# Kernel optimization log

Hardware: AMD Instinct MI355X
Metric: run time of the kernel (lower is better)

## Reference

```python
import jax, jax.numpy as jnp
import numpy as np

N, E = 10000, 320000
NF, HF = 256, 256  # input_nf/output_nf, hidden_nf
EPS = 1e-8


def setup_inputs() -> dict:
    key = jax.random.key(0)
    ks = jax.random.split(key, 20)
    h = jax.random.normal(ks[0], (N, NF), jnp.float32)
    coord = jax.random.normal(ks[1], (N, 3), jnp.float32)
    edge_index = jax.random.randint(ks[2], (2, E), 0, N, jnp.int32)

    def dense(k, fan_in, fan_out, scale=None):
        s = scale if scale is not None else 1.0 / np.sqrt(fan_in)
        W = jax.random.normal(k, (fan_in, fan_out), jnp.float32) * s
        b = jnp.zeros((fan_out,), jnp.float32)
        return W, b

    We1, be1 = dense(ks[3], 2 * NF + 1, HF)   # edge_mlp layer 1
    We2, be2 = dense(ks[4], HF, HF)           # edge_mlp layer 2
    Wn1, bn1 = dense(ks[5], HF + NF, HF)      # node_mlp layer 1
    Wn2, bn2 = dense(ks[6], HF, NF)           # node_mlp layer 2
    Wc1, bc1 = dense(ks[7], HF, HF)           # coord_mlp layer 1
    Wc2, bc2 = dense(ks[8], HF, 1, scale=0.001)  # coord_mlp final, tiny init (xavier gain=0.001)
    return dict(h=h, coord=coord, edge_index=edge_index,
                We1=We1, be1=be1, We2=We2, be2=be2,
                Wn1=Wn1, bn1=bn1, Wn2=Wn2, bn2=bn2,
                Wc1=Wc1, bc1=bc1, Wc2=Wc2, bc2=bc2)


def _segment_sum(data, seg_ids, num_segments):
    return jax.ops.segment_sum(data, seg_ids, num_segments=num_segments)


def reference(h, coord, edge_index, We1, be1, We2, be2, Wn1, bn1, Wn2, bn2, Wc1, bc1, Wc2, bc2):
    row, col = edge_index[0], edge_index[1]

    # coord2radial
    coord_diff = coord[row] - coord[col]                    # [E, 3]
    radial = jnp.sum(coord_diff ** 2, axis=1, keepdims=True)  # [E, 1]

    # edge model: MLP on [h_i, h_j, ||x_i - x_j||^2]
    edge_in = jnp.concatenate([h[row], h[col], radial], axis=1)  # [E, 2*NF+1]
    e = jax.nn.silu(edge_in @ We1 + be1)
    edge_feat = jax.nn.silu(e @ We2 + be2)                  # [E, HF]

    # coord model: coord_diff * coord_mlp(edge_feat), mean-aggregated
    c = jax.nn.silu(edge_feat @ Wc1 + bc1)
    trans = coord_diff * (c @ Wc2 + bc2)                    # [E, 3]
    agg_c = _segment_sum(trans, row, coord.shape[0])
    count = _segment_sum(jnp.ones_like(trans), row, coord.shape[0])
    coord_out = coord + agg_c / jnp.clip(count, 1.0)

    # node model: sum-aggregate edge features, concat with h, MLP
    agg_h = _segment_sum(edge_feat, row, h.shape[0])        # [N, HF]
    node_in = jnp.concatenate([h, agg_h], axis=1)           # [N, HF+NF]
    n = jax.nn.silu(node_in @ Wn1 + bn1)
    h_out = n @ Wn2 + bn2                                   # [N, NF]

    return h_out, coord_out
```

## Files before the change

### kernel.cpp

```cpp
#include <hip/hip_runtime.h>
#include <hip/hip_bf16.h>

typedef __bf16 bf16;
typedef __attribute__((ext_vector_type(8))) __bf16 bf16x8;
typedef __attribute__((ext_vector_type(4))) float f32x4;

static_assert(sizeof(bf16x8) == 16, "bf16x8 must be 16B");

constexpr int N_NODES = 10000;
constexpr int N_EDGES = 320000;
constexpr int KPAD    = 264;

__device__ __forceinline__ float silu_f(float x) { return x / (1.0f + __expf(-x)); }

__device__ __forceinline__ unsigned pk_bf16(float lo, float hi) {
  unsigned r;
  asm("v_cvt_pk_bf16_f32 %0, %1, %2" : "=v"(r) : "v"(lo), "v"(hi));
  return r;
}

__device__ __forceinline__ void mfmaT_k256(const bf16* __restrict__ WT, int wstride, int koff,
                                           const bf16* Albs, int w, int r, int q, f32x4 acc[4][4]) {
  for (int k0 = 0; k0 < 256; k0 += 32) {
    bf16x8 a[4], b[4];
#pragma unroll
    for (int mi = 0; mi < 4; ++mi)
      a[mi] = *(const bf16x8*)(WT + (size_t)(w * 64 + 16 * mi + r) * wstride + koff + k0 + q * 8);
#pragma unroll
    for (int ni = 0; ni < 4; ++ni)
      b[ni] = *(const bf16x8*)(Albs + (16 * ni + r) * KPAD + k0 + q * 8);
#pragma unroll
    for (int mi = 0; mi < 4; ++mi)
#pragma unroll
      for (int ni = 0; ni < 4; ++ni)
        acc[mi][ni] = __builtin_amdgcn_mfma_f32_16x16x32_bf16(a[mi], b[ni], acc[mi][ni], 0, 0, 0);
  }
}

__global__ __launch_bounds__(256) void prep_kernel(
    const float* __restrict__ h, const float* __restrict__ We1, const float* __restrict__ We2,
    const float* __restrict__ Wn1, const float* __restrict__ Wn2, const float* __restrict__ Wc1,
    const int* __restrict__ eidx,
    bf16* __restrict__ Hb, bf16* __restrict__ We1T, bf16* __restrict__ Wn1T,
    bf16* __restrict__ We2T, bf16* __restrict__ Wn2T, bf16* __restrict__ Wc1T,
    int* __restrict__ hist) {
  int bid = blockIdx.x, tid = threadIdx.x;
  if (bid < 10000) { int i = bid * 256 + tid; Hb[i] = (bf16)h[i]; return; }
  if (bid >= 11792) {
    int e = (bid - 11792) * 256 + tid;
    if (e < N_EDGES) atomicAdd(&hist[eidx[e]], 1);
    return;
  }
  int t = (bid - 10000) * 256 + tid;
  if (t < 131072) { int k = t >> 8, j = t & 255; We1T[j * 512 + k] = (bf16)We1[k * 256 + j]; return; }
  t -= 131072;
  if (t < 131072) { int k = t >> 8, j = t & 255; Wn1T[j * 512 + k] = (bf16)Wn1[k * 256 + j]; return; }
  t -= 131072;
  if (t < 65536) { int k = t >> 8, j = t & 255; We2T[j * 256 + k] = (bf16)We2[k * 256 + j]; return; }
  t -= 65536;
  if (t < 65536) { int k = t >> 8, j = t & 255; Wn2T[j * 256 + k] = (bf16)Wn2[k * 256 + j]; return; }
  t -= 65536;
  if (t < 65536) { int k = t >> 8, j = t & 255; Wc1T[j * 256 + k] = (bf16)Wc1[k * 256 + j]; return; }
}

__global__ __launch_bounds__(256) void scan_kernel(const int* __restrict__ hist,
                                                   int* __restrict__ base, int* __restrict__ cursor) {
  __shared__ int partial[256];
  int t = threadIdx.x;
  int s = 0;
  for (int i = 0; i < 40; ++i) { int idx = t * 40 + i; if (idx < N_NODES) s += hist[idx]; }
  partial[t] = s;
  __syncthreads();
  for (int d = 1; d < 256; d <<= 1) {
    int v = (t >= d) ? partial[t - d] : 0;
    __syncthreads();
    partial[t] += v;
    __syncthreads();
  }
  int run = partial[t] - s;
  for (int i = 0; i < 40; ++i) {
    int idx = t * 40 + i;
    if (idx < N_NODES) { base[idx] = run; cursor[idx] = run; run += hist[idx]; }
  }
}

__global__ __launch_bounds__(256) void scatter_kernel(const int* __restrict__ eidx, int* __restrict__ cursor,
                                                      int* __restrict__ rs, int* __restrict__ cs) {
  int e = blockIdx.x * 256 + threadIdx.x;
  if (e < N_EDGES) {
    int r = eidx[e], c = eidx[N_EDGES + e];
    int p = atomicAdd(&cursor[r], 1);
    rs[p] = r; cs[p] = c;
  }
}

__global__ __launch_bounds__(256, 2) void gemm_pq(const bf16* __restrict__ Hb,
                                                  const bf16* __restrict__ We1T,
                                                  const float* __restrict__ be1,
                                                  bf16* __restrict__ P, bf16* __restrict__ Q) {
  int tid = threadIdx.x, w = tid >> 6, lane = tid & 63, r = lane & 15, q = lane >> 4;
  int m0 = blockIdx.x * 64;
  int koff = blockIdx.y ? 256 : 0;
  bf16* OUT = blockIdx.y ? Q : P;
  bool addb = (blockIdx.y == 0);
  f32x4 acc[4][4];
#pragma unroll
  for (int mi = 0; mi < 4; ++mi)
#pragma unroll
    for (int ni = 0; ni < 4; ++ni) acc[mi][ni] = (f32x4){0.f, 0.f, 0.f, 0.f};

  for (int k0 = 0; k0 < 256; k0 += 32) {
    bf16x8 a[4], b[4];
#pragma unroll
    for (int mi = 0; mi < 4; ++mi)
      a[mi] = *(const bf16x8*)(We1T + (size_t)(w * 64 + 16 * mi + r) * 512 + koff + k0 + q * 8);
#pragma unroll
    for (int ni = 0; ni < 4; ++ni) {
      int m = m0 + 16 * ni + r; if (m > N_NODES - 1) m = N_NODES - 1;
      b[ni] = *(const bf16x8*)(Hb + (size_t)m * 256 + k0 + q * 8);
    }
#pragma unroll
    for (int mi = 0; mi < 4; ++mi)
#pragma unroll
      for (int ni = 0; ni < 4; ++ni)
        acc[mi][ni] = __builtin_amdgcn_mfma_f32_16x16x32_bf16(a[mi], b[ni], acc[mi][ni], 0, 0, 0);
  }
#pragma unroll
  for (int mi = 0; mi < 4; ++mi) {
    int ch = w * 64 + 16 * mi + 4 * q;
    float4 bv = addb ? *(const float4*)(be1 + ch) : (float4){0.f, 0.f, 0.f, 0.f};
#pragma unroll
    for (int ni = 0; ni < 4; ++ni) {
      int m = m0 + 16 * ni + r;
      if (m < N_NODES) {
        uint2 o;
        o.x = pk_bf16(acc[mi][ni][0] + bv.x, acc[mi][ni][1] + bv.y);
        o.y = pk_bf16(acc[mi][ni][2] + bv.z, acc[mi][ni][3] + bv.w);
        *(uint2*)(OUT + (size_t)m * 256 + ch) = o;
      }
    }
  }
}

__global__ __launch_bounds__(256, 4) void edge_kernel(
    const float* __restrict__ coord, const int* __restrict__ rs, const int* __restrict__ cs,
    const float* __restrict__ We1,
    const float* __restrict__ be2, const float* __restrict__ bc1,
    const float* __restrict__ Wc2, const float* __restrict__ bc2,
    const bf16* __restrict__ P, const bf16* __restrict__ Q,
    const bf16* __restrict__ We2T, const bf16* __restrict__ Wc1T,
    float* __restrict__ agg_h, float* __restrict__ agg_c) {
  __shared__ __align__(16) bf16 buf[64 * KPAD];
  __shared__ int s_row[64], s_col[64];
  __shared__ float s_rad[64], s_cd[64][3], s_part[64][4], s_scal[64];
  __shared__ int s_rs[65];
  __shared__ int s_nrun;

  int tid = threadIdx.x;
  int e0 = blockIdx.x * 64;
  int w = tid >> 6, lane = tid & 63, r = lane & 15, q = lane >> 4;

  if (tid < 64) {
    int e = e0 + tid;
    int ri = rs[e], ci = cs[e];
    s_row[tid] = ri; s_col[tid] = ci;
    float dx = coord[3 * ri + 0] - coord[3 * ci + 0];
    float dy = coord[3 * ri + 1] - coord[3 * ci + 1];
    float dz = coord[3 * ri + 2] - coord[3 * ci + 2];
    s_cd[tid][0] = dx; s_cd[tid][1] = dy; s_cd[tid][2] = dz;
    s_rad[tid] = dx * dx + dy * dy + dz * dz;
  }
  __syncthreads();

  if (tid < 64) {
    bool bnd = (tid == 0) || (s_row[tid] != s_row[tid - 1]);
    unsigned long long m = __ballot(bnd);
    int rank = __popcll(m & ((1ull << tid) - 1ull));
    if (bnd) s_rs[rank] = tid;
    if (tid == 0) { int R = __popcll(m); s_nrun = R; s_rs[R] = 64; }
  }

  {
    int off = (tid & 31) * 8;
    int esub = tid >> 5;
    float4 wa = *(const float4*)(We1 + 512 * 256 + off);
    float4 wb = *(const float4*)(We1 + 512 * 256 + off + 4);
#pragma unroll
    for (int p = 0; p < 8; ++p) {
      int e = p * 8 + esub;
      int ri = s_row[e], ci = s_col[e];
      bf16x8 pv = *(const bf16x8*)(P + (size_t)ri * 256 + off);
      bf16x8 qv = *(const bf16x8*)(Q + (size_t)ci * 256 + off);
      float rad = s_rad[e];
      float f0 = silu_f((float)pv[0] + (float)qv[0] + rad * wa.x);
      float f1 = silu_f((float)pv[1] + (float)qv[1] + rad * wa.y);
      float f2 = silu_f((float)pv[2] + (float)qv[2] + rad * wa.z);
      float f3 = silu_f((float)pv[3] + (float)qv[3] + rad * wa.w);
      float f4 = silu_f((float)pv[4] + (float)qv[4] + rad * wb.x);
      float f5 = silu_f((float)pv[5] + (float)qv[5] + rad * wb.y);
      float f6 = silu_f((float)pv[6] + (float)qv[6] + rad * wb.z);
      float f7 = silu_f((float)pv[7] + (float)qv[7] + rad * wb.w);
      uint4 o;
      o.x = pk_bf16(f0, f1); o.y = pk_bf16(f2, f3);
      o.z = pk_bf16(f4, f5); o.w = pk_bf16(f6, f7);
      *(uint4*)(buf + e * KPAD + off) = o;
    }
  }
  __syncthreads();

  {
    f32x4 acc[4][4];
#pragma unroll
    for (int mi = 0; mi < 4; ++mi)
#pragma unroll
      for (int ni = 0; ni < 4; ++ni) acc[mi][ni] = (f32x4){0.f, 0.f, 0.f, 0.f};
    mfmaT_k256(We2T, 256, 0, buf, w, r, q, acc);
    __syncthreads();
#pragma unroll
    for (int mi = 0; mi < 4; ++mi) {
      int ch = w * 64 + 16 * mi + 4 * q;
      float4 bv = *(const float4*)(be2 + ch);
#pragma unroll
      for (int ni = 0; ni < 4; ++ni) {
        int edge = 16 * ni + r;
        float f0 = silu_f(acc[mi][ni][0] + bv.x);
        float f1 = silu_f(acc[mi][ni][1] + bv.y);
        float f2 = silu_f(acc[mi][ni][2] + bv.z);
        float f3 = silu_f(acc[mi][ni][3] + bv.w);
        uint2 o; o.x = pk_bf16(f0, f1); o.y = pk_bf16(f2, f3);
        *(uint2*)(buf + edge * KPAD + ch) = o;
      }
    }
  }
  __syncthreads();

  f32x4 acc2[4][4];
#pragma unroll
  for (int mi = 0; mi < 4; ++mi)
#pragma unroll
    for (int ni = 0; ni < 4; ++ni) acc2[mi][ni] = (f32x4){0.f, 0.f, 0.f, 0.f};
  mfmaT_k256(Wc1T, 256, 0, buf, w, r, q, acc2);

  {
    int R = s_nrun;
    for (int rr = 0; rr < R; ++rr) {
      int st = s_rs[rr], en = s_rs[rr + 1];
      float s = 0.f;
      for (int e = st; e < en; ++e) s += (float)buf[e * KPAD + tid];
      atomicAdd(&agg_h[(size_t)s_row[st] * 256 + tid], s);
    }
  }

  {
    float p[4] = {0.f, 0.f, 0.f, 0.f};
#pragma unroll
    for (int mi = 0; mi < 4; ++mi) {
      int ch = w * 64 + 16 * mi + 4 * q;
      float4 bv = *(const float4*)(bc1 + ch);
      float4 wv = *(const float4*)(Wc2 + ch);
#pragma unroll
      for (int ni = 0; ni < 4; ++ni) {
        p[ni] += silu_f(acc2[mi][ni][0] + bv.x) * wv.x
               + silu_f(acc2[mi][ni][1] + bv.y) * wv.y
               + silu_f(acc2[mi][ni][2] + bv.z) * wv.z
               + silu_f(acc2[mi][ni][3] + bv.w) * wv.w;
      }
    }
#pragma unroll
    for (int ni = 0; ni < 4; ++ni) {
      float v = p[ni];
      v += __shfl_xor(v, 16, 64);
      v += __shfl_xor(v, 32, 64);
      if (q == 0) s_part[16 * ni + r][w] = v;
    }
  }
  __syncthreads();

  if (tid < 64)
    s_scal[tid] = s_part[tid][0] + s_part[tid][1] + s_part[tid][2] + s_part[tid][3] + bc2[0];
  __syncthreads();

  if (tid < 3) {
    int R = s_nrun;
    for (int rr = 0; rr < R; ++rr) {
      int st = s_rs[rr], en = s_rs[rr + 1];
      float s = 0.f;
      for (int e = st; e < en; ++e) s += s_cd[e][tid] * s_scal[e];
      atomicAdd(&agg_c[3 * s_row[st] + tid], s);
    }
  }
}

__global__ __launch_bounds__(256, 2) void node_kernel(
    const bf16* __restrict__ Hb, const float* __restrict__ agg_h,
    const int* __restrict__ hist, const float* __restrict__ coord, const float* __restrict__ agg_c,
    const bf16* __restrict__ Wn1T, const bf16* __restrict__ Wn2T,
    const float* __restrict__ bn1, const float* __restrict__ bn2,
    float* __restrict__ h_out, float* __restrict__ coord_out) {
  __shared__ __align__(16) bf16 buf[64 * KPAD];
  int tid = threadIdx.x, w = tid >> 6, lane = tid & 63, r = lane & 15, q = lane >> 4;
  int m0 = blockIdx.x * 64;

  if (tid < 64) {
    int m = m0 + tid;
    if (m < N_NODES) {
      float c = (float)hist[m]; if (c < 1.f) c = 1.f;
      coord_out[3 * m + 0] = coord[3 * m + 0] + agg_c[3 * m + 0] / c;
      coord_out[3 * m + 1] = coord[3 * m + 1] + agg_c[3 * m + 1] / c;
      coord_out[3 * m + 2] = coord[3 * m + 2] + agg_c[3 * m + 2] / c;
    }
  }

  f32x4 acc[4][4];
#pragma unroll
  for (int mi = 0; mi < 4; ++mi)
#pragma unroll
    for (int ni = 0; ni < 4; ++ni) acc[mi][ni] = (f32x4){0.f, 0.f, 0.f, 0.f};
  for (int k0 = 0; k0 < 256; k0 += 32) {
    bf16x8 a[4], b[4];
#pragma unroll
    for (int mi = 0; mi < 4; ++mi)
      a[mi] = *(const bf16x8*)(Wn1T + (size_t)(w * 64 + 16 * mi + r) * 512 + k0 + q * 8);
#pragma unroll
    for (int ni = 0; ni < 4; ++ni) {
      int m = m0 + 16 * ni + r; if (m > N_NODES - 1) m = N_NODES - 1;
      b[ni] = *(const bf16x8*)(Hb + (size_t)m * 256 + k0 + q * 8);
    }
#pragma unroll
    for (int mi = 0; mi < 4; ++mi)
#pragma unroll
      for (int ni = 0; ni < 4; ++ni)
        acc[mi][ni] = __builtin_amdgcn_mfma_f32_16x16x32_bf16(a[mi], b[ni], acc[mi][ni], 0, 0, 0);
  }
  for (int k0 = 0; k0 < 256; k0 += 32) {
    bf16x8 a[4], b[4];
#pragma unroll
    for (int mi = 0; mi < 4; ++mi)
      a[mi] = *(const bf16x8*)(Wn1T + (size_t)(w * 64 + 16 * mi + r) * 512 + 256 + k0 + q * 8);
#pragma unroll
    for (int ni = 0; ni < 4; ++ni) {
      int m = m0 + 16 * ni + r; if (m > N_NODES - 1) m = N_NODES - 1;
      const float* ap = agg_h + (size_t)m * 256 + k0 + q * 8;
      float4 u = *(const float4*)ap;
      float4 v = *(const float4*)(ap + 4);
      uint4 o;
      o.x = pk_bf16(u.x, u.y); o.y = pk_bf16(u.z, u.w);
      o.z = pk_bf16(v.x, v.y); o.w = pk_bf16(v.z, v.w);
      b[ni] = *(const bf16x8*)&o;
    }
#pragma unroll
    for (int mi = 0; mi < 4; ++mi)
#pragma unroll
      for (int ni = 0; ni < 4; ++ni)
        acc[mi][ni] = __builtin_amdgcn_mfma_f32_16x16x32_bf16(a[mi], b[ni], acc[mi][ni], 0, 0, 0);
  }
  __syncthreads();
#pragma unroll
  for (int mi = 0; mi < 4; ++mi) {
    int ch = w * 64 + 16 * mi + 4 * q;
    float4 bv = *(const float4*)(bn1 + ch);
#pragma unroll
    for (int ni = 0; ni < 4; ++ni) {
      int lm = 16 * ni + r;
      float f0 = silu_f(acc[mi][ni][0] + bv.x);
      float f1 = silu_f(acc[mi][ni][1] + bv.y);
      float f2 = silu_f(acc[mi][ni][2] + bv.z);
      float f3 = silu_f(acc[mi][ni][3] + bv.w);
      uint2 o; o.x = pk_bf16(f0, f1); o.y = pk_bf16(f2, f3);
      *(uint2*)(buf + lm * KPAD + ch) = o;
    }
  }
  __syncthreads();
  f32x4 acc2[4][4];
#pragma unroll
  for (int mi = 0; mi < 4; ++mi)
#pragma unroll
    for (int ni = 0; ni < 4; ++ni) acc2[mi][ni] = (f32x4){0.f, 0.f, 0.f, 0.f};
  mfmaT_k256(Wn2T, 256, 0, buf, w, r, q, acc2);
#pragma unroll
  for (int mi = 0; mi < 4; ++mi) {
    int ch = w * 64 + 16 * mi + 4 * q;
    float4 bv = *(const float4*)(bn2 + ch);
#pragma unroll
    for (int ni = 0; ni < 4; ++ni) {
      int m = m0 + 16 * ni + r;
      if (m < N_NODES) {
        float4 o;
        o.x = acc2[mi][ni][0] + bv.x;
        o.y = acc2[mi][ni][1] + bv.y;
        o.z = acc2[mi][ni][2] + bv.z;
        o.w = acc2[mi][ni][3] + bv.w;
        *(float4*)(h_out + (size_t)m * 256 + ch) = o;
      }
    }
  }
}

extern "C" void kernel_launch(void* const* d_in, const int* in_sizes, int n_in,
                              void* d_out, int out_size, void* d_ws, size_t ws_size,
                              hipStream_t stream) {
  const float* h     = (const float*)d_in[0];
  const float* coord = (const float*)d_in[1];
  const int*   eidx  = (const int*)d_in[2];
  const float* We1 = (const float*)d_in[3];
  const float* be1 = (const float*)d_in[4];
  const float* We2 = (const float*)d_in[5];
  const float* be2 = (const float*)d_in[6];
  const float* Wn1 = (const float*)d_in[7];
  const float* bn1 = (const float*)d_in[8];
  const float* Wn2 = (const float*)d_in[9];
  const float* bn2 = (const float*)d_in[10];
  const float* Wc1 = (const float*)d_in[11];
  const float* bc1 = (const float*)d_in[12];
  const float* Wc2 = (const float*)d_in[13];
  const float* bc2 = (const float*)d_in[14];

  char* ws = (char*)d_ws;
  float* agg_h = (float*)(ws + 0);
  float* agg_c = (float*)(ws + 10240000);
  int*   hist  = (int*)  (ws + 10360000);
  int*   base  = (int*)  (ws + 10400000);
  int*   cursor= (int*)  (ws + 10440000);
  int*   rs    = (int*)  (ws + 10480000);
  int*   cs    = (int*)  (ws + 11760000);
  bf16* Hb   = (bf16*)(ws + 13040000);
  bf16* P    = (bf16*)(ws + 18160000);
  bf16* Q    = (bf16*)(ws + 23280000);
  bf16* We1T = (bf16*)(ws + 28400000);
  bf16* Wn1T = (bf16*)(ws + 28662144);
  bf16* We2T = (bf16*)(ws + 28924288);
  bf16* Wn2T = (bf16*)(ws + 29055360);
  bf16* Wc1T = (bf16*)(ws + 29186432);

  float* h_out = (float*)d_out;
  float* coord_out = h_out + (size_t)N_NODES * 256;

  hipMemsetAsync(ws, 0, 10400000, stream);
  prep_kernel<<<13042, 256, 0, stream>>>(h, We1, We2, Wn1, Wn2, Wc1, eidx,
                                         Hb, We1T, Wn1T, We2T, Wn2T, Wc1T, hist);
  scan_kernel<<<1, 256, 0, stream>>>(hist, base, cursor);
  scatter_kernel<<<1250, 256, 0, stream>>>(eidx, cursor, rs, cs);
  gemm_pq<<<dim3(157, 2), 256, 0, stream>>>(Hb, We1T, be1, P, Q);
  edge_kernel<<<5000, 256, 0, stream>>>(coord, rs, cs, We1, be2, bc1, Wc2, bc2,
                                        P, Q, We2T, Wc1T, agg_h, agg_c);
  node_kernel<<<157, 256, 0, stream>>>(Hb, agg_h, hist, coord, agg_c,
                                       Wn1T, Wn2T, bn1, bn2, h_out, coord_out);
}
```

Baseline: 444.1 us.

## Shrink node GEMM tiles, vectorize weight transpose, fuse zeroing into prep

The node-side GEMMs (gemm_pq and node_kernel) now use 16-row tiles across 625 blocks instead of 64-row tiles across 157, so they fill more CUs on a 10000-node problem. Weight transposes write packed 8-element bf16 vectors. The large agg_h/agg_c memset moves into the prep kernel as float4 stores. The row/col arrays are packed into one int2 array. The scan stages hist in shared memory. SiLU uses a hardware reciprocal. Smaller tiles reduce weight reuse per block, and the bf16 transpose reads are strided.

```diff
diff --git a/kernel.cpp b/kernel.cpp
--- a/kernel.cpp
+++ b/kernel.cpp
@@ -11,7 +11,10 @@
 constexpr int N_EDGES = 320000;
 constexpr int KPAD    = 264;
 
-__device__ __forceinline__ float silu_f(float x) { return x / (1.0f + __expf(-x)); }
+__device__ __forceinline__ float rcp_f(float x) {
+  float r; asm("v_rcp_f32 %0, %1" : "=v"(r) : "v"(x)); return r;
+}
+__device__ __forceinline__ float silu_f(float x) { return x * rcp_f(1.0f + __expf(-x)); }
 
 __device__ __forceinline__ unsigned pk_bf16(float lo, float hi) {
   unsigned r;
@@ -35,6 +38,39 @@
       for (int ni = 0; ni < 4; ++ni)
         acc[mi][ni] = __builtin_amdgcn_mfma_f32_16x16x32_bf16(a[mi], b[ni], acc[mi][ni], 0, 0, 0);
   }
+}
+
+__device__ __forceinline__ void mfmaT_k256_b1(const bf16* __restrict__ WT, int wstride, int koff,
+                                              const bf16* Albs, int w, int r, int q, f32x4 acc[4]) {
+  for (int k0 = 0; k0 < 256; k0 += 32) {
+    bf16x8 a[4], b;
+    b = *(const bf16x8*)(Albs + r * KPAD + k0 + q * 8);
+#pragma unroll
+    for (int mi = 0; mi < 4; ++mi)
+      a[mi] = *(const bf16x8*)(WT + (size_t)(w * 64 + 16 * mi + r) * wstride + koff + k0 + q * 8);
+#pragma unroll
+    for (int mi = 0; mi < 4; ++mi)
+      acc[mi] = __builtin_amdgcn_mfma_f32_16x16x32_bf16(a[mi], b, acc[mi], 0, 0, 0);
+  }
+}
+
+__device__ __forceinline__ void transpose512(const float* __restrict__ W, bf16* __restrict__ WT,
+                                             int local, int tid) {
+  int tg = local * 256 + tid;
+  int j = tg >> 6, k0 = (tg & 63) * 8;
+  bf16x8 v;
+#pragma unroll
+  for (int i = 0; i < 8; ++i) v[i] = (bf16)W[(size_t)(k0 + i) * 256 + j];
+  *(bf16x8*)(WT + (size_t)j * 512 + k0) = v;
+}
+__device__ __forceinline__ void transpose256(const float* __restrict__ W, bf16* __restrict__ WT,
+                                             int local, int tid) {
+  int tg = local * 256 + tid;
+  int j = tg >> 5, k0 = (tg & 31) * 8;
+  bf16x8 v;
+#pragma unroll
+  for (int i = 0; i < 8; ++i) v[i] = (bf16)W[(size_t)(k0 + i) * 256 + j];
+  *(bf16x8*)(WT + (size_t)j * 256 + k0) = v;
 }
 
 __global__ __launch_bounds__(256) void prep_kernel(
@@ -43,32 +79,37 @@
     const int* __restrict__ eidx,
     bf16* __restrict__ Hb, bf16* __restrict__ We1T, bf16* __restrict__ Wn1T,
     bf16* __restrict__ We2T, bf16* __restrict__ Wn2T, bf16* __restrict__ Wc1T,
-    int* __restrict__ hist) {
+    int* __restrict__ hist, float4* __restrict__ zero_base) {
   int bid = blockIdx.x, tid = threadIdx.x;
   if (bid < 10000) { int i = bid * 256 + tid; Hb[i] = (bf16)h[i]; return; }
-  if (bid >= 11792) {
-    int e = (bid - 11792) * 256 + tid;
+  if (bid < 10224) {
+    int wb = bid - 10000;
+    if (wb < 64)       transpose512(We1, We1T, wb, tid);
+    else if (wb < 128) transpose512(Wn1, Wn1T, wb - 64, tid);
+    else if (wb < 160) transpose256(We2, We2T, wb - 128, tid);
+    else if (wb < 192) transpose256(Wn2, Wn2T, wb - 160, tid);
+    else               transpose256(Wc1, Wc1T, wb - 192, tid);
+    return;
+  }
+  if (bid < 11474) {
+    int e = (bid - 11474 + 1250) * 256 + tid - 1250 * 256;
+    e = (bid - 10224) * 256 + tid;
     if (e < N_EDGES) atomicAdd(&hist[eidx[e]], 1);
     return;
   }
-  int t = (bid - 10000) * 256 + tid;
-  if (t < 131072) { int k = t >> 8, j = t & 255; We1T[j * 512 + k] = (bf16)We1[k * 256 + j]; return; }
-  t -= 131072;
-  if (t < 131072) { int k = t >> 8, j = t & 255; Wn1T[j * 512 + k] = (bf16)Wn1[k * 256 + j]; return; }
-  t -= 131072;
-  if (t < 65536) { int k = t >> 8, j = t & 255; We2T[j * 256 + k] = (bf16)We2[k * 256 + j]; return; }
-  t -= 65536;
-  if (t < 65536) { int k = t >> 8, j = t & 255; Wn2T[j * 256 + k] = (bf16)Wn2[k * 256 + j]; return; }
-  t -= 65536;
-  if (t < 65536) { int k = t >> 8, j = t & 255; Wc1T[j * 256 + k] = (bf16)Wc1[k * 256 + j]; return; }
+  int z = (bid - 11474) * 256 + tid;
+  if (z < 647500) zero_base[z] = (float4){0.f, 0.f, 0.f, 0.f};
 }
 
 __global__ __launch_bounds__(256) void scan_kernel(const int* __restrict__ hist,
                                                    int* __restrict__ base, int* __restrict__ cursor) {
+  __shared__ int sh[10000];
   __shared__ int partial[256];
   int t = threadIdx.x;
+  for (int i = 0; i < 40; ++i) { int idx = i * 256 + t; if (idx < N_NODES) sh[idx] = hist[idx]; }
+  __syncthreads();
   int s = 0;
-  for (int i = 0; i < 40; ++i) { int idx = t * 40 + i; if (idx < N_NODES) s += hist[idx]; }
+  for (int i = 0; i < 40; ++i) { int idx = t * 40 + i; if (idx < N_NODES) s += sh[idx]; }
   partial[t] = s;
   __syncthreads();
   for (int d = 1; d < 256; d <<= 1) {
@@ -80,17 +121,22 @@
   int run = partial[t] - s;
   for (int i = 0; i < 40; ++i) {
     int idx = t * 40 + i;
-    if (idx < N_NODES) { base[idx] = run; cursor[idx] = run; run += hist[idx]; }
+    if (idx < N_NODES) { int hv = sh[idx]; sh[idx] = run; run += hv; }
+  }
+  __syncthreads();
+  for (int i = 0; i < 40; ++i) {
+    int idx = i * 256 + t;
+    if (idx < N_NODES) { int v = sh[idx]; base[idx] = v; cursor[idx] = v; }
   }
 }
 
 __global__ __launch_bounds__(256) void scatter_kernel(const int* __restrict__ eidx, int* __restrict__ cursor,
-                                                      int* __restrict__ rs, int* __restrict__ cs) {
+                                                      int2* __restrict__ rc) {
   int e = blockIdx.x * 256 + threadIdx.x;
   if (e < N_EDGES) {
     int r = eidx[e], c = eidx[N_EDGES + e];
     int p = atomicAdd(&cursor[r], 1);
-    rs[p] = r; cs[p] = c;
+    rc[p] = (int2){r, c};
   }
 }
 
@@ -99,51 +145,38 @@
                                                   const float* __restrict__ be1,
                                                   bf16* __restrict__ P, bf16* __restrict__ Q) {
   int tid = threadIdx.x, w = tid >> 6, lane = tid & 63, r = lane & 15, q = lane >> 4;
-  int m0 = blockIdx.x * 64;
+  int m0 = blockIdx.x * 16;
   int koff = blockIdx.y ? 256 : 0;
   bf16* OUT = blockIdx.y ? Q : P;
   bool addb = (blockIdx.y == 0);
-  f32x4 acc[4][4];
-#pragma unroll
-  for (int mi = 0; mi < 4; ++mi)
-#pragma unroll
-    for (int ni = 0; ni < 4; ++ni) acc[mi][ni] = (f32x4){0.f, 0.f, 0.f, 0.f};
+  f32x4 acc[4];
+#pragma unroll
+  for (int mi = 0; mi < 4; ++mi) acc[mi] = (f32x4){0.f, 0.f, 0.f, 0.f};
+  int m = m0 + r;
 
   for (int k0 = 0; k0 < 256; k0 += 32) {
-    bf16x8 a[4], b[4];
+    bf16x8 a[4], b;
+    b = *(const bf16x8*)(Hb + (size_t)m * 256 + k0 + q * 8);
 #pragma unroll
     for (int mi = 0; mi < 4; ++mi)
       a[mi] = *(const bf16x8*)(We1T + (size_t)(w * 64 + 16 * mi + r) * 512 + koff + k0 + q * 8);
 #pragma unroll
-    for (int ni = 0; ni < 4; ++ni) {
-      int m = m0 + 16 * ni + r; if (m > N_NODES - 1) m = N_NODES - 1;
-      b[ni] = *(const bf16x8*)(Hb + (size_t)m * 256 + k0 + q * 8);
-    }
-#pragma unroll
-    for (int mi = 0; mi < 4; ++mi)
-#pragma unroll
-      for (int ni = 0; ni < 4; ++ni)
-        acc[mi][ni] = __builtin_amdgcn_mfma_f32_16x16x32_bf16(a[mi], b[ni], acc[mi][ni], 0, 0, 0);
+    for (int mi = 0; mi < 4; ++mi)
+      acc[mi] = __builtin_amdgcn_mfma_f32_16x16x32_bf16(a[mi], b, acc[mi], 0, 0, 0);
   }
 #pragma unroll
   for (int mi = 0; mi < 4; ++mi) {
     int ch = w * 64 + 16 * mi + 4 * q;
     float4 bv = addb ? *(const float4*)(be1 + ch) : (float4){0.f, 0.f, 0.f, 0.f};
-#pragma unroll
-    for (int ni = 0; ni < 4; ++ni) {
-      int m = m0 + 16 * ni + r;
-      if (m < N_NODES) {
-        uint2 o;
-        o.x = pk_bf16(acc[mi][ni][0] + bv.x, acc[mi][ni][1] + bv.y);
-        o.y = pk_bf16(acc[mi][ni][2] + bv.z, acc[mi][ni][3] + bv.w);
-        *(uint2*)(OUT + (size_t)m * 256 + ch) = o;
-      }
-    }
+    uint2 o;
+    o.x = pk_bf16(acc[mi][0] + bv.x, acc[mi][1] + bv.y);
+    o.y = pk_bf16(acc[mi][2] + bv.z, acc[mi][3] + bv.w);
+    *(uint2*)(OUT + (size_t)m * 256 + ch) = o;
   }
 }
 
 __global__ __launch_bounds__(256, 4) void edge_kernel(
-    const float* __restrict__ coord, const int* __restrict__ rs, const int* __restrict__ cs,
+    const float* __restrict__ coord, const int2* __restrict__ rc,
     const float* __restrict__ We1,
     const float* __restrict__ be2, const float* __restrict__ bc1,
     const float* __restrict__ Wc2, const float* __restrict__ bc2,
@@ -161,8 +194,8 @@
   int w = tid >> 6, lane = tid & 63, r = lane & 15, q = lane >> 4;
 
   if (tid < 64) {
-    int e = e0 + tid;
-    int ri = rs[e], ci = cs[e];
+    int2 v = rc[e0 + tid];
+    int ri = v.x, ci = v.y;
     s_row[tid] = ri; s_col[tid] = ci;
     float dx = coord[3 * ri + 0] - coord[3 * ci + 0];
     float dy = coord[3 * ri + 1] - coord[3 * ci + 1];
@@ -297,102 +330,77 @@
     const bf16* __restrict__ Wn1T, const bf16* __restrict__ Wn2T,
     const float* __restrict__ bn1, const float* __restrict__ bn2,
     float* __restrict__ h_out, float* __restrict__ coord_out) {
-  __shared__ __align__(16) bf16 buf[64 * KPAD];
+  __shared__ __align__(16) bf16 buf[16 * KPAD];
   int tid = threadIdx.x, w = tid >> 6, lane = tid & 63, r = lane & 15, q = lane >> 4;
-  int m0 = blockIdx.x * 64;
-
-  if (tid < 64) {
-    int m = m0 + tid;
-    if (m < N_NODES) {
-      float c = (float)hist[m]; if (c < 1.f) c = 1.f;
-      coord_out[3 * m + 0] = coord[3 * m + 0] + agg_c[3 * m + 0] / c;
-      coord_out[3 * m + 1] = coord[3 * m + 1] + agg_c[3 * m + 1] / c;
-      coord_out[3 * m + 2] = coord[3 * m + 2] + agg_c[3 * m + 2] / c;
-    }
-  }
-
-  f32x4 acc[4][4];
-#pragma unroll
-  for (int mi = 0; mi < 4; ++mi)
-#pragma unroll
-    for (int ni = 0; ni < 4; ++ni) acc[mi][ni] = (f32x4){0.f, 0.f, 0.f, 0.f};
+  int m0 = blockIdx.x * 16;
+  int m = m0 + r;
+
+  if (tid < 16) {
+    int mm = m0 + tid;
+    float c = (float)hist[mm]; if (c < 1.f) c = 1.f;
+    coord_out[3 * mm + 0] = coord[3 * mm + 0] + agg_c[3 * mm + 0] / c;
+    coord_out[3 * mm + 1] = coord[3 * mm + 1] + agg_c[3 * mm + 1] / c;
+    coord_out[3 * mm + 2] = coord[3 * mm + 2] + agg_c[3 * mm + 2] / c;
+  }
+
+  f32x4 acc[4];
+#pragma unroll
+  for (int mi = 0; mi < 4; ++mi) acc[mi] = (f32x4){0.f, 0.f, 0.f, 0.f};
   for (int k0 = 0; k0 < 256; k0 += 32) {
-    bf16x8 a[4], b[4];
+    bf16x8 a[4], b;
+    b = *(const bf16x8*)(Hb + (size_t)m * 256 + k0 + q * 8);
 #pragma unroll
     for (int mi = 0; mi < 4; ++mi)
       a[mi] = *(const bf16x8*)(Wn1T + (size_t)(w * 64 + 16 * mi + r) * 512 + k0 + q * 8);
 #pragma unroll
-    for (int ni = 0; ni < 4; ++ni) {
-      int m = m0 + 16 * ni + r; if (m > N_NODES - 1) m = N_NODES - 1;
-      b[ni] = *(const bf16x8*)(Hb + (size_t)m * 256 + k0 + q * 8);
-    }
-#pragma unroll
-    for (int mi = 0; mi < 4; ++mi)
-#pragma unroll
-      for (int ni = 0; ni < 4; ++ni)
-        acc[mi][ni] = __builtin_amdgcn_mfma_f32_16x16x32_bf16(a[mi], b[ni], acc[mi][ni], 0, 0, 0);
+    for (int mi = 0; mi < 4; ++mi)
+      acc[mi] = __builtin_amdgcn_mfma_f32_16x16x32_bf16(a[mi], b, acc[mi], 0, 0, 0);
   }
   for (int k0 = 0; k0 < 256; k0 += 32) {
-    bf16x8 a[4], b[4];
-#pragma unroll
-    for (int mi = 0; mi < 4; ++mi)
-      a[mi] = *(const bf16x8*)(Wn1T + (size_t)(w * 64 + 16 * mi + r) * 512 + 256 + k0 + q * 8);
-#pragma unroll
-    for (int ni = 0; ni < 4; ++ni) {
-      int m = m0 + 16 * ni + r; if (m > N_NODES - 1) m = N_NODES - 1;
+    bf16x8 a[4], b;
+    {
       const float* ap = agg_h + (size_t)m * 256 + k0 + q * 8;
       float4 u = *(const float4*)ap;
       float4 v = *(const float4*)(ap + 4);
       uint4 o;
       o.x = pk_bf16(u.x, u.y); o.y = pk_bf16(u.z, u.w);
       o.z = pk_bf16(v.x, v.y); o.w = pk_bf16(v.z, v.w);
-      b[ni] = *(const bf16x8*)&o;
-    }
-#pragma unroll
-    for (int mi = 0; mi < 4; ++mi)
-#pragma unroll
-      for (int ni = 0; ni < 4; ++ni)
-        acc[mi][ni] = __builtin_amdgcn_mfma_f32_16x16x32_bf16(a[mi], b[ni], acc[mi][ni], 0, 0, 0);
+      b = *(const bf16x8*)&o;
+    }
+#pragma unroll
+    for (int mi = 0; mi < 4; ++mi)
+      a[mi] = *(const bf16x8*)(Wn1T + (size_t)(w * 64 + 16 * mi + r) * 512 + 256 + k0 + q * 8);
+#pragma unroll
+    for (int mi = 0; mi < 4; ++mi)
+      acc[mi] = __builtin_amdgcn_mfma_f32_16x16x32_bf16(a[mi], b, acc[mi], 0, 0, 0);
   }
   __syncthreads();
 #pragma unroll
   for (int mi = 0; mi < 4; ++mi) {
     int ch = w * 64 + 16 * mi + 4 * q;
     float4 bv = *(const float4*)(bn1 + ch);
-#pragma unroll
-    for (int ni = 0; ni < 4; ++ni) {
-      int lm = 16 * ni + r;
-      float f0 = silu_f(acc[mi][ni][0] + bv.x);
-      float f1 = silu_f(acc[mi][ni][1] + bv.y);
-      float f2 = silu_f(acc[mi][ni][2] + bv.z);
-      float f3 = silu_f(acc[mi][ni][3] + bv.w);
-      uint2 o; o.x = pk_bf16(f0, f1); o.y = pk_bf16(f2, f3);
-      *(uint2*)(buf + lm * KPAD + ch) = o;
-    }
-  }
-  __syncthreads();
-  f32x4 acc2[4][4];
-#pragma unroll
-  for (int mi = 0; mi < 4; ++mi)
-#pragma unroll
-    for (int ni = 0; ni < 4; ++ni) acc2[mi][ni] = (f32x4){0.f, 0.f, 0.f, 0.f};
-  mfmaT_k256(Wn2T, 256, 0, buf, w, r, q, acc2);
+    float f0 = silu_f(acc[mi][0] + bv.x);
+    float f1 = silu_f(acc[mi][1] + bv.y);
+    float f2 = silu_f(acc[mi][2] + bv.z);
+    float f3 = silu_f(acc[mi][3] + bv.w);
+    uint2 o; o.x = pk_bf16(f0, f1); o.y = pk_bf16(f2, f3);
+    *(uint2*)(buf + r * KPAD + ch) = o;
+  }
+  __syncthreads();
+  f32x4 acc2[4];
+#pragma unroll
+  for (int mi = 0; mi < 4; ++mi) acc2[mi] = (f32x4){0.f, 0.f, 0.f, 0.f};
+  mfmaT_k256_b1(Wn2T, 256, 0, buf, w, r, q, acc2);
 #pragma unroll
   for (int mi = 0; mi < 4; ++mi) {
     int ch = w * 64 + 16 * mi + 4 * q;
     float4 bv = *(const float4*)(bn2 + ch);
-#pragma unroll
-    for (int ni = 0; ni < 4; ++ni) {
-      int m = m0 + 16 * ni + r;
-      if (m < N_NODES) {
-        float4 o;
-        o.x = acc2[mi][ni][0] + bv.x;
-        o.y = acc2[mi][ni][1] + bv.y;
-        o.z = acc2[mi][ni][2] + bv.z;
-        o.w = acc2[mi][ni][3] + bv.w;
-        *(float4*)(h_out + (size_t)m * 256 + ch) = o;
-      }
-    }
+    float4 o;
+    o.x = acc2[mi][0] + bv.x;
+    o.y = acc2[mi][1] + bv.y;
+    o.z = acc2[mi][2] + bv.z;
+    o.w = acc2[mi][3] + bv.w;
+    *(float4*)(h_out + (size_t)m * 256 + ch) = o;
   }
 }
 
@@ -421,8 +429,7 @@
   int*   hist  = (int*)  (ws + 10360000);
   int*   base  = (int*)  (ws + 10400000);
   int*   cursor= (int*)  (ws + 10440000);
-  int*   rs    = (int*)  (ws + 10480000);
-  int*   cs    = (int*)  (ws + 11760000);
+  int2*  rc    = (int2*) (ws + 10480000);
   bf16* Hb   = (bf16*)(ws + 13040000);
   bf16* P    = (bf16*)(ws + 18160000);
   bf16* Q    = (bf16*)(ws + 23280000);
@@ -435,14 +442,15 @@
   float* h_out = (float*)d_out;
   float* coord_out = h_out + (size_t)N_NODES * 256;
 
-  hipMemsetAsync(ws, 0, 10400000, stream);
-  prep_kernel<<<13042, 256, 0, stream>>>(h, We1, We2, Wn1, Wn2, Wc1, eidx,
-                                         Hb, We1T, Wn1T, We2T, Wn2T, Wc1T, hist);
+  hipMemsetAsync(hist, 0, 40000, stream);
+  prep_kernel<<<14014, 256, 0, stream>>>(h, We1, We2, Wn1, Wn2, Wc1, eidx,
+                                         Hb, We1T, Wn1T, We2T, Wn2T, Wc1T, hist,
+                                         (float4*)agg_h);
   scan_kernel<<<1, 256, 0, stream>>>(hist, base, cursor);
-  scatter_kernel<<<1250, 256, 0, stream>>>(eidx, cursor, rs, cs);
-  gemm_pq<<<dim3(157, 2), 256, 0, stream>>>(Hb, We1T, be1, P, Q);
-  edge_kernel<<<5000, 256, 0, stream>>>(coord, rs, cs, We1, be2, bc1, Wc2, bc2,
+  scatter_kernel<<<1250, 256, 0, stream>>>(eidx, cursor, rc);
+  gemm_pq<<<dim3(625, 2), 256, 0, stream>>>(Hb, We1T, be1, P, Q);
+  edge_kernel<<<5000, 256, 0, stream>>>(coord, rc, We1, be2, bc1, Wc2, bc2,
                                         P, Q, We2T, Wc1T, agg_h, agg_c);
-  node_kernel<<<157, 256, 0, stream>>>(Hb, agg_h, hist, coord, agg_c,
+  node_kernel<<<625, 256, 0, stream>>>(Hb, agg_h, hist, coord, agg_c,
                                        Wn1T, Wn2T, bn1, bn2, h_out, coord_out);
 }
```

After: 409.0 us. 1.09x faster.
